# Kernel tuning notes

Hardware: AMD Instinct MI355X
Metric: run time of the kernel (lower is better)

Reference implementation:

```python
import jax, jax.numpy as jnp
import numpy as np

D_MODEL = 2048
NUM_HEADS = 16
HEAD_DIM = D_MODEL // NUM_HEADS  # 128


def setup_inputs() -> dict:
    key = jax.random.key(0)
    ks = jax.random.split(key, 11)
    B, S = 2, 2048
    s = 0.02
    return {
        "q": jax.random.normal(ks[0], (B, S, D_MODEL), jnp.float32),
        "k": jax.random.normal(ks[1], (B, S, D_MODEL), jnp.float32),
        "v": jax.random.normal(ks[2], (B, S, D_MODEL), jnp.float32),
        "Wq": jax.random.normal(ks[3], (D_MODEL, D_MODEL), jnp.float32) * s,
        "bq": jnp.zeros((D_MODEL,), jnp.float32),
        "Wk": jax.random.normal(ks[4], (D_MODEL, HEAD_DIM), jnp.float32) * s,
        "bk": jnp.zeros((HEAD_DIM,), jnp.float32),
        "Wv": jax.random.normal(ks[5], (D_MODEL, HEAD_DIM), jnp.float32) * s,
        "bv": jnp.zeros((HEAD_DIM,), jnp.float32),
        "Wo": jax.random.normal(ks[6], (D_MODEL, D_MODEL), jnp.float32) * s,
        "bo": jnp.zeros((D_MODEL,), jnp.float32),
    }


def reference(q, k, v, Wq, bq, Wk, bk, Wv, bv, Wo, bo):
    B, Sq, _ = q.shape
    Skv = k.shape[1]
    # Query projection -> per-head queries [B, H, Sq, Dh]
    qh = (q @ Wq + bq).reshape(B, Sq, NUM_HEADS, HEAD_DIM).transpose(0, 2, 1, 3)
    # Shared single-head K/V projections [B, Skv, Dh]
    kh = k @ Wk + bk
    vh = v @ Wv + bv
    scale = 1.0 / jnp.sqrt(jnp.asarray(HEAD_DIM, qh.dtype))
    # MQA: broadcast shared K over heads without materializing per-head copies
    scores = jnp.einsum("bhqd,bkd->bhqk", qh, kh) * scale  # [B, H, Sq, Skv]
    attn = jax.nn.softmax(scores, axis=-1)
    out = jnp.einsum("bhqk,bkd->bhqd", attn, vh)  # [B, H, Sq, Dh]
    out = out.transpose(0, 2, 1, 3).reshape(B, Sq, D_MODEL)
    return out @ Wo + bo
```

## Files before the change

### kernel.cpp

```cpp
#include <hip/hip_runtime.h>

typedef unsigned short u16;
typedef unsigned int u32;
typedef __bf16 bf16_t;
typedef __attribute__((ext_vector_type(8))) bf16_t bf16x8;
typedef __attribute__((ext_vector_type(4))) float f32x4;
typedef __attribute__((ext_vector_type(16))) float f32x16;
typedef __attribute__((ext_vector_type(2))) unsigned int u32x2;

__device__ inline u16 f2bf(float f) {
    union { float f; u32 u; } v; v.f = f;
    u32 u = v.u;
    u32 r = (u + 0x7fffu + ((u >> 16) & 1u)) >> 16;
    return (u16)r;
}

__device__ inline u32 cvt_pk_bf16(float lo, float hi) {
    u32 r;
    asm("v_cvt_pk_bf16_f32 %0, %1, %2" : "=v"(r) : "v"(lo), "v"(hi));
    return r;
}

__device__ inline void async_cp16(const void* g, void* l) {
    __builtin_amdgcn_global_load_lds((const __attribute__((address_space(1))) void*)g,
                                     (__attribute__((address_space(3))) void*)l, 16, 0, 0);
}

__global__ __launch_bounds__(256) void cvt3(const float* __restrict__ a,
                                            const float* __restrict__ b,
                                            const float* __restrict__ c,
                                            u16* __restrict__ oa, u16* __restrict__ ob,
                                            u16* __restrict__ oc) {
    int z = blockIdx.y;
    const float* in = z == 0 ? a : (z == 1 ? b : c);
    u16* out = z == 0 ? oa : (z == 1 ? ob : oc);
    int i = (blockIdx.x * 256 + threadIdx.x) * 4;
    float4 f = *(const float4*)(in + i);
    ushort4 o;
    o.x = f2bf(f.x); o.y = f2bf(f.y); o.z = f2bf(f.z); o.w = f2bf(f.w);
    *(ushort4*)(out + i) = o;
}

__global__ __launch_bounds__(256) void transpose2(const float* __restrict__ W0,
                                                  u16* __restrict__ T0,
                                                  const float* __restrict__ W1,
                                                  u16* __restrict__ T1,
                                                  int K, int N) {
    const float* W = blockIdx.z == 0 ? W0 : W1;
    u16* WT = blockIdx.z == 0 ? T0 : T1;
    __shared__ float tile[32][33];
    int tr0 = blockIdx.x * 32;
    int tc0 = blockIdx.y * 32;
    int t = threadIdx.x;
    for (int i = 0; i < 4; i++) {
        int idx = t + i * 256; int r = idx >> 5, c = idx & 31;
        tile[r][c] = W[(size_t)(tr0 + r) * N + tc0 + c];
    }
    __syncthreads();
    for (int i = 0; i < 4; i++) {
        int idx = t + i * 256; int r = idx >> 5, c = idx & 31;
        WT[(size_t)(tc0 + r) * K + tr0 + c] = f2bf(tile[c][r]);
    }
}

template <typename OUT_T>
__global__ __launch_bounds__(512, 2) void gemm_bt2(const u16* __restrict__ A,
                                                   const u16* __restrict__ BT,
                                                   const float* __restrict__ bias,
                                                   OUT_T* __restrict__ C,
                                                   int M, int N, int K, int ldout) {
    __shared__ u16 smem[3 * 24576];
    int t = threadIdx.x, lane = t & 63, wv = t >> 6;
    int quad = lane >> 4, c16 = lane & 15;
    int rx = c16 & 7;
    int wr = wv >> 1, wc = wv & 1;

    int bid = blockIdx.x;
    int xcd = bid & 7;
    int loc = bid >> 3;
    int bm = (((xcd >> 1) << 2) + (loc & 3)) << 8;
    int bn = (((xcd & 1) << 3) + (loc >> 2)) << 7;

    f32x4 acc[4][4] = {};

    int srow = wv * 8 + (lane >> 3);
    int scol = ((lane & 7) ^ (lane >> 3)) * 8;
    const u16* Ag = A + (size_t)(bm + srow) * K + scol;
    const u16* Bg = BT + (size_t)(bn + srow) * K + scol;

    auto STAGE = [&](int kt, int d) {
        u16* base = smem + d * 24576;
        u16* ad = base + (size_t)(wv * 8) * 64;
        u16* bd = base + 16384 + (size_t)(wv * 8) * 64;
        const u16* ag = Ag + (size_t)kt * 64;
        const u16* bg = Bg + (size_t)kt * 64;
        for (int p = 0; p < 4; p++)
            async_cp16(ag + (size_t)(p * 64) * K, ad + p * 4096);
        for (int p = 0; p < 2; p++)
            async_cp16(bg + (size_t)(p * 64) * K, bd + p * 4096);
    };

    const int NT = K >> 6;
    STAGE(0, 0);
    STAGE(1, 1);

    for (int tt = 0; tt < NT; tt++) {
        if (tt + 1 < NT) asm volatile("s_waitcnt vmcnt(6)" ::: "memory");
        else             asm volatile("s_waitcnt vmcnt(0)" ::: "memory");
        __builtin_amdgcn_s_barrier();
        if (tt + 2 < NT) STAGE(tt + 2, (tt + 2) % 3);

        const u16* sA = smem + (tt % 3) * 24576;
        const u16* sB = sA + 16384;

        for (int rh = 0; rh < 2; rh++) {
            bf16x8 af[2][2];
            for (int mi = 0; mi < 2; mi++)
                for (int kk = 0; kk < 2; kk++)
                    af[mi][kk] = *(const bf16x8*)&sA[(wr * 64 + rh * 32 + mi * 16 + c16) * 64 +
                                                     (((kk * 4 + quad) ^ rx) * 8)];
            for (int ch = 0; ch < 2; ch++) {
                bf16x8 bf[2][2];
                for (int ni = 0; ni < 2; ni++)
                    for (int kk = 0; kk < 2; kk++)
                        bf[ni][kk] = *(const bf16x8*)&sB[(wc * 64 + ch * 32 + ni * 16 + c16) * 64 +
                                                         (((kk * 4 + quad) ^ rx) * 8)];
                __builtin_amdgcn_s_setprio(1);
                for (int kk = 0; kk < 2; kk++)
                    for (int mi = 0; mi < 2; mi++)
                        for (int ni = 0; ni < 2; ni++)
                            acc[rh * 2 + mi][ch * 2 + ni] = __builtin_amdgcn_mfma_f32_16x16x32_bf16(
                                af[mi][kk], bf[ni][kk], acc[rh * 2 + mi][ch * 2 + ni], 0, 0, 0);
                __builtin_amdgcn_s_setprio(0);
            }
        }
    }

    for (int mi = 0; mi < 4; mi++) {
        for (int ni = 0; ni < 4; ni++) {
            int col = bn + wc * 64 + ni * 16 + c16;
            float bv = bias[col];
            for (int p = 0; p < 4; p++) {
                int row = bm + wr * 64 + mi * 16 + quad * 4 + p;
                float v = acc[mi][ni][p] + bv;
                size_t off = (size_t)row * ldout + col;
                if constexpr (__is_same(OUT_T, u16)) C[off] = f2bf(v);
                else C[off] = v;
            }
        }
    }
}

__global__ __launch_bounds__(256) void gemm_kv_sk(const u16* __restrict__ kbf,
                                                  const u16* __restrict__ vbf,
                                                  const u16* __restrict__ WkT,
                                                  const u16* __restrict__ WvT,
                                                  float* __restrict__ kacc,
                                                  float* __restrict__ vacc,
                                                  int K, int KS) {
    bool isv = blockIdx.y == 1;
    const u16* A = isv ? vbf : kbf;
    const u16* BT = isv ? WvT : WkT;
    float* aco = isv ? vacc : kacc;
    __shared__ u16 sA[128 * 32];
    __shared__ u16 sB[128 * 32];
    int t = threadIdx.x, lane = t & 63, wv = t >> 6;
    int quad = lane >> 4, c16 = lane & 15;
    int bm = blockIdx.x * 128;
    int wm = (wv & 1) * 64, wn = (wv >> 1) * 64;
    f32x4 acc[4][4] = {};

    int srow = wv * 32 + (lane >> 2);
    int scol = (lane & 3) * 8;
    const u16* Ag = A + (size_t)(bm + srow) * K + scol;
    const u16* Bg = BT + (size_t)srow * K + scol;
    u16* sAd = &sA[(wv * 32) * 32];
    u16* sBd = &sB[(wv * 32) * 32];

    int kbeg = blockIdx.z * KS;
    for (int k0 = kbeg; k0 < kbeg + KS; k0 += 32) {
        __syncthreads();
        async_cp16(Ag + k0, sAd);
        async_cp16(Ag + (size_t)16 * K + k0, sAd + 16 * 32);
        async_cp16(Bg + k0, sBd);
        async_cp16(Bg + (size_t)16 * K + k0, sBd + 16 * 32);
        __syncthreads();
        bf16x8 af[4], bfr[4];
        for (int mi = 0; mi < 4; mi++)
            af[mi] = *(const bf16x8*)&sA[(wm + mi * 16 + c16) * 32 + quad * 8];
        for (int ni = 0; ni < 4; ni++)
            bfr[ni] = *(const bf16x8*)&sB[(wn + ni * 16 + c16) * 32 + quad * 8];
        for (int mi = 0; mi < 4; mi++)
            for (int ni = 0; ni < 4; ni++)
                acc[mi][ni] = __builtin_amdgcn_mfma_f32_16x16x32_bf16(
                    af[mi], bfr[ni], acc[mi][ni], 0, 0, 0);
    }

    for (int mi = 0; mi < 4; mi++)
        for (int ni = 0; ni < 4; ni++) {
            int col = wn + ni * 16 + c16;
            for (int p = 0; p < 4; p++) {
                int row = bm + wm + mi * 16 + quad * 4 + p;
                atomicAdd(&aco[(size_t)row * 128 + col], acc[mi][ni][p]);
            }
        }
}

__global__ __launch_bounds__(256) void cvt_kv(const float* __restrict__ kacc,
                                              const float* __restrict__ vacc,
                                              const float* __restrict__ bk,
                                              const float* __restrict__ bv,
                                              u16* __restrict__ khb,
                                              u16* __restrict__ vhT,
                                              int M) {
    int t = threadIdx.x;
    int tr0 = blockIdx.x * 32;
    int tc0 = blockIdx.y * 32;
    if (blockIdx.z == 0) {
        for (int i = 0; i < 4; i++) {
            int idx = t + i * 256; int r = idx >> 5, c = idx & 31;
            khb[(size_t)(tr0 + r) * 128 + tc0 + c] =
                f2bf(kacc[(size_t)(tr0 + r) * 128 + tc0 + c] + bk[tc0 + c]);
        }
    } else {
        __shared__ float tile[32][33];
        for (int i = 0; i < 4; i++) {
            int idx = t + i * 256; int r = idx >> 5, c = idx & 31;
            tile[r][c] = vacc[(size_t)(tr0 + r) * 128 + tc0 + c] + bv[tc0 + c];
        }
        __syncthreads();
        for (int i = 0; i < 4; i++) {
            int idx = t + i * 256; int r = idx >> 5, c = idx & 31;
            vhT[(size_t)(tc0 + r) * M + tr0 + c] = f2bf(tile[c][r]);
        }
    }
}

__global__ __launch_bounds__(256, 2) void mqa_attn(const u16* __restrict__ qh,
                                                   const u16* __restrict__ kh,
                                                   const u16* __restrict__ vhT,
                                                   u16* __restrict__ outp,
                                                   int S) {
    constexpr float CEXP = 0.08838834764831845f * 1.4426950408889634f;
    __shared__ u16 smem[32768];
    u16* sK0 = smem;
    u16* sV0 = smem + 16384;

    int t = threadIdx.x, lane = t & 63, wv = t >> 6;
    int l31 = lane & 31, hh = lane >> 5;
    int lx = l31 & 7;
    int b = blockIdx.z, hb = blockIdx.y;
    int q0w = blockIdx.x * 128 + wv * 32;
    int BS = b * S;

    bf16x8 aq[8];
    {
        const u16* qp = qh + (size_t)(BS + q0w + l31) * 2048 + hb * 128 + hh * 8;
#pragma unroll
        for (int st = 0; st < 8; st++) aq[st] = *(const bf16x8*)(qp + st * 16);
    }

    f32x16 accO[4] = {};
    float lsum = 0.f;

    int ksub = lane >> 4, kch = lane & 15;
    int klx = (wv * 4 + ksub) & 7;
    const u16* kgb = kh + (size_t)(BS + wv * 4 + ksub) * 128 + ((kch ^ klx) * 8);
    int vsub = lane >> 3, vch = lane & 7;
    int vlx = vsub & 7;
    const u16* vgb = vhT + (size_t)(wv * 8 + vsub) * 4096 + BS + ((vch ^ vlx) * 8);

    u16* kb0 = sK0 + (wv * 4) * 128;
    u16* vb0 = sV0 + (wv * 8) * 64;

    auto STAGE = [&](int kv0, int d) {
        u16* kb = kb0 + d * 8192;
        u16* vb = vb0 + d * 8192;
        for (int p = 0; p < 4; p++)
            async_cp16(kgb + (size_t)(kv0 + p * 16) * 128, kb + p * 2048);
        for (int p = 0; p < 4; p++)
            async_cp16(vgb + (size_t)(p * 32) * 4096 + kv0, vb + p * 2048);
    };

    const int NT = S >> 6;
    STAGE(0, 0);
    __syncthreads();

    for (int tt = 0; tt < NT; tt++) {
        int cur = tt & 1;
        if (tt + 1 < NT) STAGE((tt + 1) * 64, cur ^ 1);
        const u16* sKc = sK0 + cur * 8192;
        const u16* sVc = sV0 + cur * 8192;

        bf16x8 pf[4];
#pragma unroll
        for (int sub = 0; sub < 2; sub++) {
            f32x16 accS = {};
            const u16* krow = sKc + (size_t)(sub * 32 + l31) * 128;
#pragma unroll
            for (int st = 0; st < 8; st++) {
                bf16x8 kf = *(const bf16x8*)(krow + (((st * 2 + hh) ^ lx) * 8));
                accS = __builtin_amdgcn_mfma_f32_32x32x16_bf16(kf, aq[st], accS, 0, 0, 0);
            }
            u32 P[8];
#pragma unroll
            for (int g = 0; g < 4; g++) {
                float e0 = __builtin_amdgcn_exp2f(accS[4 * g + 0] * CEXP);
                float e1 = __builtin_amdgcn_exp2f(accS[4 * g + 1] * CEXP);
                float e2 = __builtin_amdgcn_exp2f(accS[4 * g + 2] * CEXP);
                float e3 = __builtin_amdgcn_exp2f(accS[4 * g + 3] * CEXP);
                P[2 * g] = cvt_pk_bf16(e0, e1);
                P[2 * g + 1] = cvt_pk_bf16(e2, e3);
            }
#pragma unroll
            for (int w = 0; w < 8; w++) {
                union { u32 u; float f; } lo, hi;
                lo.u = P[w] << 16;
                hi.u = P[w] & 0xffff0000u;
                lsum += lo.f + hi.f;
            }
            u32x2 a0 = __builtin_amdgcn_permlane32_swap(P[0], P[2], false, false);
            u32x2 a1 = __builtin_amdgcn_permlane32_swap(P[1], P[3], false, false);
            u32x2 a2 = __builtin_amdgcn_permlane32_swap(P[4], P[6], false, false);
            u32x2 a3 = __builtin_amdgcn_permlane32_swap(P[5], P[7], false, false);
            union { u32 u[4]; bf16x8 v; } f0, f1;
            f0.u[0] = a0.x; f0.u[1] = a1.x; f0.u[2] = a0.y; f0.u[3] = a1.y;
            f1.u[0] = a2.x; f1.u[1] = a3.x; f1.u[2] = a2.y; f1.u[3] = a3.y;
            pf[sub * 2] = f0.v;
            pf[sub * 2 + 1] = f1.v;
        }

#pragma unroll
        for (int db = 0; db < 4; db++) {
            const u16* vrow = sVc + (size_t)(db * 32 + l31) * 64;
#pragma unroll
            for (int ks = 0; ks < 4; ks++) {
                bf16x8 vf = *(const bf16x8*)(vrow + (((ks * 2 + hh) ^ lx) * 8));
                accO[db] = __builtin_amdgcn_mfma_f32_32x32x16_bf16(pf[ks], vf, accO[db], 0, 0, 0);
            }
        }

        __syncthreads();
    }

    lsum += __shfl_xor(lsum, 32, 64);
    float invq = 1.f / lsum;
    float inv[16];
#pragma unroll
    for (int r = 0; r < 16; r++) {
        int qloc = (r & 3) + 8 * (r >> 2) + 4 * hh;
        inv[r] = __shfl(invq, qloc, 64);
    }
#pragma unroll
    for (int db = 0; db < 4; db++) {
#pragma unroll
        for (int r = 0; r < 16; r++) {
            int qloc = (r & 3) + 8 * (r >> 2) + 4 * hh;
            outp[(size_t)(BS + q0w + qloc) * 2048 + hb * 128 + db * 32 + l31] =
                f2bf(accO[db][r] * inv[r]);
        }
    }
}

extern "C" void kernel_launch(void* const* d_in, const int* in_sizes, int n_in,
                              void* d_out, int out_size, void* d_ws, size_t ws_size,
                              hipStream_t stream) {
    const float* q  = (const float*)d_in[0];
    const float* k  = (const float*)d_in[1];
    const float* v  = (const float*)d_in[2];
    const float* Wq = (const float*)d_in[3];
    const float* bq = (const float*)d_in[4];
    const float* Wk = (const float*)d_in[5];
    const float* bk = (const float*)d_in[6];
    const float* Wv = (const float*)d_in[7];
    const float* bv = (const float*)d_in[8];
    const float* Wo = (const float*)d_in[9];
    const float* bo = (const float*)d_in[10];
    float* out = (float*)d_out;

    const int S = 2048, D = 2048, Dh = 128, M = 4096;
    const int QKV = M * D;
    const int WDD = D * D;
    const int WDH = D * Dh;
    const int MDh = M * Dh;

    u16* ws   = (u16*)d_ws;
    u16* q_bf = ws;
    u16* k_bf = q_bf + QKV;
    u16* v_bf = k_bf + QKV;
    u16* WqT  = v_bf + QKV;
    u16* WoT  = WqT + WDD;
    u16* WkT  = WoT + WDD;
    u16* WvT  = WkT + WDH;
    u16* qhb  = WvT + WDH;
    u16* khb  = qhb + QKV;
    u16* vhTb = khb + MDh;
    u16* aout = vhTb + MDh;
    float* kacc = (float*)(aout + QKV);
    float* vacc = kacc + MDh;

    hipMemsetAsync(kacc, 0, (size_t)2 * MDh * sizeof(float), stream);

    cvt3<<<dim3(QKV / 1024, 3), 256, 0, stream>>>(q, k, v, q_bf, k_bf, v_bf);
    transpose2<<<dim3(64, 64, 2), 256, 0, stream>>>(Wq, WqT, Wo, WoT, D, D);
    transpose2<<<dim3(64, 4, 2), 256, 0, stream>>>(Wk, WkT, Wv, WvT, D, Dh);

    gemm_bt2<u16><<<dim3(256), 512, 0, stream>>>(q_bf, WqT, bq, qhb, M, D, D, D);
    gemm_kv_sk<<<dim3(32, 2, 4), 256, 0, stream>>>(k_bf, v_bf, WkT, WvT, kacc, vacc, D, 512);
    cvt_kv<<<dim3(128, 4, 2), 256, 0, stream>>>(kacc, vacc, bk, bv, khb, vhTb, M);

    mqa_attn<<<dim3(16, 16, 2), 256, 0, stream>>>(qhb, khb, vhTb, aout, S);

    gemm_bt2<float><<<dim3(256), 512, 0, stream>>>(aout, WoT, bo, out, M, D, D, D);
}
```

Baseline: 361.3 us.

## Split KV tile across wave pairs, each wave handling two query tiles

Waves are regrouped so each pair of waves shares 64 queries, and each wave covers half of every 64-key tile for two 32-query subtiles. Each K/V fragment read from LDS is reused for two MFMAs, which halves LDS traffic per MFMA. The two halves' partial outputs and row sums are combined through shared memory at the end. The second query tile is reloaded from global memory on every iteration instead of being held in registers, and the row sum now accumulates the unrounded fp32 exponentials. This raises register pressure and adds a reduction epilogue.

```diff
diff --git a/kernel.cpp b/kernel.cpp
--- a/kernel.cpp
+++ b/kernel.cpp
@@ -242,26 +242,30 @@
                                                    u16* __restrict__ outp,
                                                    int S) {
     constexpr float CEXP = 0.08838834764831845f * 1.4426950408889634f;
-    __shared__ u16 smem[32768];
+    __shared__ u16 smem[33024];
     u16* sK0 = smem;
     u16* sV0 = smem + 16384;
 
     int t = threadIdx.x, lane = t & 63, wv = t >> 6;
     int l31 = lane & 31, hh = lane >> 5;
     int lx = l31 & 7;
+    int qs = wv >> 1, kvh = wv & 1;
     int b = blockIdx.z, hb = blockIdx.y;
-    int q0w = blockIdx.x * 128 + wv * 32;
+    int q0w = blockIdx.x * 128 + qs * 64;
     int BS = b * S;
 
-    bf16x8 aq[8];
+    bf16x8 aq0[8];
+    const u16* qp1;
     {
-        const u16* qp = qh + (size_t)(BS + q0w + l31) * 2048 + hb * 128 + hh * 8;
-#pragma unroll
-        for (int st = 0; st < 8; st++) aq[st] = *(const bf16x8*)(qp + st * 16);
-    }
-
-    f32x16 accO[4] = {};
-    float lsum = 0.f;
+        const u16* qp0 = qh + (size_t)(BS + q0w + l31) * 2048 + hb * 128 + hh * 8;
+#pragma unroll
+        for (int st = 0; st < 8; st++) aq0[st] = *(const bf16x8*)(qp0 + st * 16);
+        qp1 = qh + (size_t)(BS + q0w + 32 + l31) * 2048 + hb * 128 + hh * 8;
+    }
+
+    f32x16 accO0[4] = {};
+    f32x16 accO1[4] = {};
+    float lsum0 = 0.f, lsum1 = 0.f;
 
     int ksub = lane >> 4, kch = lane & 15;
     int klx = (wv * 4 + ksub) & 7;
@@ -282,6 +286,28 @@
             async_cp16(vgb + (size_t)(p * 32) * 4096 + kv0, vb + p * 2048);
     };
 
+    auto SOFTMAX = [&](const f32x16& accS, float& ls, bf16x8& pfa, bf16x8& pfb) {
+        u32 P[8];
+#pragma unroll
+        for (int g = 0; g < 4; g++) {
+            float e0 = __builtin_amdgcn_exp2f(accS[4 * g + 0] * CEXP);
+            float e1 = __builtin_amdgcn_exp2f(accS[4 * g + 1] * CEXP);
+            float e2 = __builtin_amdgcn_exp2f(accS[4 * g + 2] * CEXP);
+            float e3 = __builtin_amdgcn_exp2f(accS[4 * g + 3] * CEXP);
+            ls += (e0 + e1) + (e2 + e3);
+            P[2 * g] = cvt_pk_bf16(e0, e1);
+            P[2 * g + 1] = cvt_pk_bf16(e2, e3);
+        }
+        u32x2 a0 = __builtin_amdgcn_permlane32_swap(P[0], P[2], false, false);
+        u32x2 a1 = __builtin_amdgcn_permlane32_swap(P[1], P[3], false, false);
+        u32x2 a2 = __builtin_amdgcn_permlane32_swap(P[4], P[6], false, false);
+        u32x2 a3 = __builtin_amdgcn_permlane32_swap(P[5], P[7], false, false);
+        union { u32 u[4]; bf16x8 v; } f0, f1;
+        f0.u[0] = a0.x; f0.u[1] = a1.x; f0.u[2] = a0.y; f0.u[3] = a1.y;
+        f1.u[0] = a2.x; f1.u[1] = a3.x; f1.u[2] = a2.y; f1.u[3] = a3.y;
+        pfa = f0.v; pfb = f1.v;
+    };
+
     const int NT = S >> 6;
     STAGE(0, 0);
     __syncthreads();
@@ -292,73 +318,82 @@
         const u16* sKc = sK0 + cur * 8192;
         const u16* sVc = sV0 + cur * 8192;
 
-        bf16x8 pf[4];
-#pragma unroll
-        for (int sub = 0; sub < 2; sub++) {
-            f32x16 accS = {};
-            const u16* krow = sKc + (size_t)(sub * 32 + l31) * 128;
-#pragma unroll
-            for (int st = 0; st < 8; st++) {
-                bf16x8 kf = *(const bf16x8*)(krow + (((st * 2 + hh) ^ lx) * 8));
-                accS = __builtin_amdgcn_mfma_f32_32x32x16_bf16(kf, aq[st], accS, 0, 0, 0);
-            }
-            u32 P[8];
-#pragma unroll
-            for (int g = 0; g < 4; g++) {
-                float e0 = __builtin_amdgcn_exp2f(accS[4 * g + 0] * CEXP);
-                float e1 = __builtin_amdgcn_exp2f(accS[4 * g + 1] * CEXP);
-                float e2 = __builtin_amdgcn_exp2f(accS[4 * g + 2] * CEXP);
-                float e3 = __builtin_amdgcn_exp2f(accS[4 * g + 3] * CEXP);
-                P[2 * g] = cvt_pk_bf16(e0, e1);
-                P[2 * g + 1] = cvt_pk_bf16(e2, e3);
-            }
-#pragma unroll
-            for (int w = 0; w < 8; w++) {
-                union { u32 u; float f; } lo, hi;
-                lo.u = P[w] << 16;
-                hi.u = P[w] & 0xffff0000u;
-                lsum += lo.f + hi.f;
-            }
-            u32x2 a0 = __builtin_amdgcn_permlane32_swap(P[0], P[2], false, false);
-            u32x2 a1 = __builtin_amdgcn_permlane32_swap(P[1], P[3], false, false);
-            u32x2 a2 = __builtin_amdgcn_permlane32_swap(P[4], P[6], false, false);
-            u32x2 a3 = __builtin_amdgcn_permlane32_swap(P[5], P[7], false, false);
-            union { u32 u[4]; bf16x8 v; } f0, f1;
-            f0.u[0] = a0.x; f0.u[1] = a1.x; f0.u[2] = a0.y; f0.u[3] = a1.y;
-            f1.u[0] = a2.x; f1.u[1] = a3.x; f1.u[2] = a2.y; f1.u[3] = a3.y;
-            pf[sub * 2] = f0.v;
-            pf[sub * 2 + 1] = f1.v;
-        }
+        f32x16 accS0 = {}, accS1 = {};
+        const u16* krow = sKc + (size_t)(kvh * 32 + l31) * 128;
+#pragma unroll
+        for (int st = 0; st < 8; st++) {
+            bf16x8 kf = *(const bf16x8*)(krow + (((st * 2 + hh) ^ lx) * 8));
+            bf16x8 a1 = *(const bf16x8*)(qp1 + st * 16);
+            accS0 = __builtin_amdgcn_mfma_f32_32x32x16_bf16(kf, aq0[st], accS0, 0, 0, 0);
+            accS1 = __builtin_amdgcn_mfma_f32_32x32x16_bf16(kf, a1, accS1, 0, 0, 0);
+        }
+
+        bf16x8 pf0[2], pf1[2];
+        SOFTMAX(accS0, lsum0, pf0[0], pf0[1]);
+        SOFTMAX(accS1, lsum1, pf1[0], pf1[1]);
 
 #pragma unroll
         for (int db = 0; db < 4; db++) {
             const u16* vrow = sVc + (size_t)(db * 32 + l31) * 64;
 #pragma unroll
-            for (int ks = 0; ks < 4; ks++) {
-                bf16x8 vf = *(const bf16x8*)(vrow + (((ks * 2 + hh) ^ lx) * 8));
-                accO[db] = __builtin_amdgcn_mfma_f32_32x32x16_bf16(pf[ks], vf, accO[db], 0, 0, 0);
+            for (int ks = 0; ks < 2; ks++) {
+                bf16x8 vf = *(const bf16x8*)(vrow + (((kvh * 4 + ks * 2 + hh) ^ lx) * 8));
+                accO0[db] = __builtin_amdgcn_mfma_f32_32x32x16_bf16(pf0[ks], vf, accO0[db], 0, 0, 0);
+                accO1[db] = __builtin_amdgcn_mfma_f32_32x32x16_bf16(pf1[ks], vf, accO1[db], 0, 0, 0);
             }
         }
 
         __syncthreads();
     }
 
-    lsum += __shfl_xor(lsum, 32, 64);
-    float invq = 1.f / lsum;
-    float inv[16];
-#pragma unroll
-    for (int r = 0; r < 16; r++) {
-        int qloc = (r & 3) + 8 * (r >> 2) + 4 * hh;
-        inv[r] = __shfl(invq, qloc, 64);
-    }
-#pragma unroll
-    for (int db = 0; db < 4; db++) {
-#pragma unroll
-        for (int r = 0; r < 16; r++) {
-            int qloc = (r & 3) + 8 * (r >> 2) + 4 * hh;
-            outp[(size_t)(BS + q0w + qloc) * 2048 + hb * 128 + db * 32 + l31] =
-                f2bf(accO[db][r] * inv[r]);
-        }
+    float xs[2];
+    {
+        float x0 = lsum0 + __shfl_xor(lsum0, 32, 64);
+        float x1 = lsum1 + __shfl_xor(lsum1, 32, 64);
+        xs[0] = x0; xs[1] = x1;
+    }
+    float* sComb = (float*)smem;
+    float* sL = (float*)(smem + 32768);
+
+#pragma unroll
+    for (int g = 0; g < 2; g++) {
+        const f32x16* aco = (g == 0) ? accO0 : accO1;
+        if (kvh == 1) {
+            if (hh == 0) sL[qs * 32 + l31] = xs[g];
+            float* dst = sComb + qs * 4096;
+#pragma unroll
+            for (int db = 0; db < 4; db++)
+#pragma unroll
+                for (int rr = 0; rr < 4; rr++) {
+                    f32x4 part;
+                    part[0] = aco[db][rr * 4 + 0];
+                    part[1] = aco[db][rr * 4 + 1];
+                    part[2] = aco[db][rr * 4 + 2];
+                    part[3] = aco[db][rr * 4 + 3];
+                    *(f32x4*)(dst + (db * 4 + rr) * 256 + lane * 4) = part;
+                }
+        }
+        __syncthreads();
+        if (kvh == 0) {
+            float ltot = xs[g] + sL[qs * 32 + l31];
+            float invq = 1.f / ltot;
+            const float* src = sComb + qs * 4096;
+#pragma unroll
+            for (int db = 0; db < 4; db++)
+#pragma unroll
+                for (int rr = 0; rr < 4; rr++) {
+                    f32x4 o = *(const f32x4*)(src + (db * 4 + rr) * 256 + lane * 4);
+#pragma unroll
+                    for (int p = 0; p < 4; p++) {
+                        int r = rr * 4 + p;
+                        int qloc = (r & 3) + 8 * (r >> 2) + 4 * hh;
+                        float v = (o[p] + aco[db][r]) * __shfl(invq, qloc, 64);
+                        outp[(size_t)(BS + q0w + g * 32 + qloc) * 2048 + hb * 128 + db * 32 + l31] =
+                            f2bf(v);
+                    }
+                }
+        }
+        __syncthreads();
     }
 }
 
```

New measurement: 367.1 us. About the same (+1.6%).

## Shrink projection GEMM tile to 128x128 with 256 threads and double buffering

Applied to the files above, without the earlier changes.

Replaces the 256x128-tile, 512-thread, triple-buffered projection GEMM with a 128x128-tile, 256-thread kernel that double-buffers with __syncthreads instead of vmcnt-based waits. The grid doubles to 512 blocks and the XCD-aware tile mapping is updated to match. Each wave now loads all A/B fragments before a single block of MFMAs. The aim is more blocks per CU and less LDS per block, at the cost of less data reuse per tile and a full barrier each k-step that exposes load latency.

```diff
diff --git a/kernel.cpp b/kernel.cpp
--- a/kernel.cpp
+++ b/kernel.cpp
@@ -64,76 +64,69 @@
 }
 
 template <typename OUT_T>
-__global__ __launch_bounds__(512, 2) void gemm_bt2(const u16* __restrict__ A,
+__global__ __launch_bounds__(256, 2) void gemm_bt3(const u16* __restrict__ A,
                                                    const u16* __restrict__ BT,
                                                    const float* __restrict__ bias,
                                                    OUT_T* __restrict__ C,
                                                    int M, int N, int K, int ldout) {
-    __shared__ u16 smem[3 * 24576];
+    __shared__ u16 smem[2 * 16384];
     int t = threadIdx.x, lane = t & 63, wv = t >> 6;
     int quad = lane >> 4, c16 = lane & 15;
     int rx = c16 & 7;
     int wr = wv >> 1, wc = wv & 1;
 
     int bid = blockIdx.x;
-    int xcd = bid & 7;
-    int loc = bid >> 3;
-    int bm = (((xcd >> 1) << 2) + (loc & 3)) << 8;
-    int bn = (((xcd & 1) << 3) + (loc >> 2)) << 7;
+    int xcd = bid & 7, loc = bid >> 3;
+    int bm = (((xcd >> 1) << 3) + (loc & 7)) << 7;
+    int bn = (((xcd & 1) << 3) + (loc >> 3)) << 7;
 
     f32x4 acc[4][4] = {};
 
     int srow = wv * 8 + (lane >> 3);
-    int scol = ((lane & 7) ^ (lane >> 3)) * 8;
+    int scol = ((lane & 7) ^ (srow & 7)) * 8;
     const u16* Ag = A + (size_t)(bm + srow) * K + scol;
     const u16* Bg = BT + (size_t)(bn + srow) * K + scol;
+    u16* ad0 = smem + (wv * 8) * 64;
+    u16* bd0 = smem + 8192 + (wv * 8) * 64;
 
     auto STAGE = [&](int kt, int d) {
-        u16* base = smem + d * 24576;
-        u16* ad = base + (size_t)(wv * 8) * 64;
-        u16* bd = base + 16384 + (size_t)(wv * 8) * 64;
+        u16* ad = ad0 + d * 16384;
+        u16* bd = bd0 + d * 16384;
         const u16* ag = Ag + (size_t)kt * 64;
         const u16* bg = Bg + (size_t)kt * 64;
         for (int p = 0; p < 4; p++)
-            async_cp16(ag + (size_t)(p * 64) * K, ad + p * 4096);
-        for (int p = 0; p < 2; p++)
-            async_cp16(bg + (size_t)(p * 64) * K, bd + p * 4096);
+            async_cp16(ag + (size_t)(p * 32) * K, ad + p * 2048);
+        for (int p = 0; p < 4; p++)
+            async_cp16(bg + (size_t)(p * 32) * K, bd + p * 2048);
     };
 
     const int NT = K >> 6;
     STAGE(0, 0);
-    STAGE(1, 1);
+    __syncthreads();
 
     for (int tt = 0; tt < NT; tt++) {
-        if (tt + 1 < NT) asm volatile("s_waitcnt vmcnt(6)" ::: "memory");
-        else             asm volatile("s_waitcnt vmcnt(0)" ::: "memory");
-        __builtin_amdgcn_s_barrier();
-        if (tt + 2 < NT) STAGE(tt + 2, (tt + 2) % 3);
-
-        const u16* sA = smem + (tt % 3) * 24576;
-        const u16* sB = sA + 16384;
-
-        for (int rh = 0; rh < 2; rh++) {
-            bf16x8 af[2][2];
-            for (int mi = 0; mi < 2; mi++)
-                for (int kk = 0; kk < 2; kk++)
-                    af[mi][kk] = *(const bf16x8*)&sA[(wr * 64 + rh * 32 + mi * 16 + c16) * 64 +
-                                                     (((kk * 4 + quad) ^ rx) * 8)];
-            for (int ch = 0; ch < 2; ch++) {
-                bf16x8 bf[2][2];
-                for (int ni = 0; ni < 2; ni++)
-                    for (int kk = 0; kk < 2; kk++)
-                        bf[ni][kk] = *(const bf16x8*)&sB[(wc * 64 + ch * 32 + ni * 16 + c16) * 64 +
-                                                         (((kk * 4 + quad) ^ rx) * 8)];
-                __builtin_amdgcn_s_setprio(1);
-                for (int kk = 0; kk < 2; kk++)
-                    for (int mi = 0; mi < 2; mi++)
-                        for (int ni = 0; ni < 2; ni++)
-                            acc[rh * 2 + mi][ch * 2 + ni] = __builtin_amdgcn_mfma_f32_16x16x32_bf16(
-                                af[mi][kk], bf[ni][kk], acc[rh * 2 + mi][ch * 2 + ni], 0, 0, 0);
-                __builtin_amdgcn_s_setprio(0);
-            }
-        }
+        int cur = tt & 1;
+        if (tt + 1 < NT) STAGE(tt + 1, cur ^ 1);
+        const u16* sA = smem + cur * 16384;
+        const u16* sB = sA + 8192;
+
+        bf16x8 af[4][2], bf[4][2];
+        for (int mi = 0; mi < 4; mi++)
+            for (int kk = 0; kk < 2; kk++)
+                af[mi][kk] = *(const bf16x8*)&sA[(wr * 64 + mi * 16 + c16) * 64 +
+                                                 (((kk * 4 + quad) ^ rx) * 8)];
+        for (int ni = 0; ni < 4; ni++)
+            for (int kk = 0; kk < 2; kk++)
+                bf[ni][kk] = *(const bf16x8*)&sB[(wc * 64 + ni * 16 + c16) * 64 +
+                                                 (((kk * 4 + quad) ^ rx) * 8)];
+        __builtin_amdgcn_s_setprio(1);
+        for (int kk = 0; kk < 2; kk++)
+            for (int mi = 0; mi < 4; mi++)
+                for (int ni = 0; ni < 4; ni++)
+                    acc[mi][ni] = __builtin_amdgcn_mfma_f32_16x16x32_bf16(
+                        af[mi][kk], bf[ni][kk], acc[mi][ni], 0, 0, 0);
+        __builtin_amdgcn_s_setprio(0);
+        __syncthreads();
     }
 
     for (int mi = 0; mi < 4; mi++) {
@@ -405,11 +398,11 @@
     transpose2<<<dim3(64, 64, 2), 256, 0, stream>>>(Wq, WqT, Wo, WoT, D, D);
     transpose2<<<dim3(64, 4, 2), 256, 0, stream>>>(Wk, WkT, Wv, WvT, D, Dh);
 
-    gemm_bt2<u16><<<dim3(256), 512, 0, stream>>>(q_bf, WqT, bq, qhb, M, D, D, D);
+    gemm_bt3<u16><<<dim3(512), 256, 0, stream>>>(q_bf, WqT, bq, qhb, M, D, D, D);
     gemm_kv_sk<<<dim3(32, 2, 4), 256, 0, stream>>>(k_bf, v_bf, WkT, WvT, kacc, vacc, D, 512);
     cvt_kv<<<dim3(128, 4, 2), 256, 0, stream>>>(kacc, vacc, bk, bv, khb, vhTb, M);
 
     mqa_attn<<<dim3(16, 16, 2), 256, 0, stream>>>(qhb, khb, vhTb, aout, S);
 
-    gemm_bt2<float><<<dim3(256), 512, 0, stream>>>(aout, WoT, bo, out, M, D, D, D);
-}
+    gemm_bt3<float><<<dim3(512), 256, 0, stream>>>(aout, WoT, bo, out, M, D, D, D);
+}
```

After: 357.1 us. No clear change (-1.2%).
